# Optimization experiments

Measured on AMD Instinct MI355X. Metric: run time of the kernel, lower is better.

The kernel has to match this reference:

```python
import jax, jax.numpy as jnp
import numpy as np

SHAPES = np.array([[64, 64], [32, 32], [16, 16], [8, 8]], dtype=np.int64)  # (H_l, W_l)
STARTS = np.array([0, 4096, 5120, 5376], dtype=np.int64)
N_HEADS, N_LEVELS, N_POINTS = 8, 4, 4
NUM_LAYERS, D_MODEL, D_FFN = 6, 256, 1024
B, S = 1, int(SHAPES[:, 0].dot(SHAPES[:, 1]).item()) if False else (1, 5440)[1]
B = 1


def setup_inputs():
    key = jax.random.key(0)
    ks = jax.random.split(key, 16)
    C, F, L = D_MODEL, D_FFN, NUM_LAYERS
    w = lambda k, shape, s: jax.random.normal(k, shape, jnp.float32) * s
    d = {}
    d["src"] = jax.random.normal(ks[0], (B, S, C), jnp.float32)
    d["pos"] = jax.random.normal(ks[1], (B, S, C), jnp.float32) * 0.1
    d["valid_ratios"] = jnp.ones((B, N_LEVELS, 2), jnp.float32)
    d["spatial_shapes"] = jnp.asarray(SHAPES)
    d["level_start_index"] = jnp.asarray(STARTS)
    d["Wv"] = w(ks[2], (L, C, C), 0.03); d["bv"] = jnp.zeros((L, C), jnp.float32)
    d["Woff"] = w(ks[3], (L, C, N_HEADS * N_LEVELS * N_POINTS * 2), 0.002)
    d["boff"] = w(ks[4], (L, N_HEADS * N_LEVELS * N_POINTS * 2), 0.5)
    d["Wattn"] = w(ks[5], (L, C, N_HEADS * N_LEVELS * N_POINTS), 0.02)
    d["battn"] = jnp.zeros((L, N_HEADS * N_LEVELS * N_POINTS), jnp.float32)
    d["Wout"] = w(ks[6], (L, C, C), 0.03); d["bout"] = jnp.zeros((L, C), jnp.float32)
    d["ln1_g"] = jnp.ones((L, C), jnp.float32); d["ln1_b"] = jnp.zeros((L, C), jnp.float32)
    d["W1"] = w(ks[7], (L, C, F), 0.03); d["b1"] = jnp.zeros((L, F), jnp.float32)
    d["W2"] = w(ks[8], (L, F, C), 0.03); d["b2"] = jnp.zeros((L, C), jnp.float32)
    d["ln2_g"] = jnp.ones((L, C), jnp.float32); d["ln2_b"] = jnp.zeros((L, C), jnp.float32)
    return d


def layer_norm(x, g, b, eps=1e-5):
    m = jnp.mean(x, -1, keepdims=True)
    v = jnp.mean(jnp.square(x - m), -1, keepdims=True)
    return (x - m) * jax.lax.rsqrt(v + eps) * g + b


def get_reference_points(valid_ratios):
    # returns [B, S, L, 2] (x, y) normalized coords, matching the TF while-loop
    refs = []
    for l in range(N_LEVELS):
        H, W = int(SHAPES[l, 0]), int(SHAPES[l, 1])
        ry = jnp.linspace(0.5, H - 0.5, H)
        rx = jnp.linspace(0.5, W - 0.5, W)
        yy, xx = jnp.meshgrid(ry, rx, indexing='ij')
        yn = yy.reshape(-1)[None, :] / (valid_ratios[:, l, 0:1] * H)
        xn = xx.reshape(-1)[None, :] / (valid_ratios[:, l, 1:2] * W)
        refs.append(jnp.stack([xn, yn], -1))  # [B, H*W, 2]
    ref = jnp.concatenate(refs, axis=1)       # [B, S, 2]
    vr_wh = valid_ratios[:, None, :, ::-1]    # [B, 1, L, 2] -> (w, h)
    return ref[:, :, None, :] * vr_wh


def bilinear_sample(v_l, loc, Hl, Wl):
    # v_l: [B, Hl*Wl, nH, Dh]; loc: [B, S, nH, P, 2] in [0,1] coords
    # grid_sample align_corners=False, zero padding: pix = loc*size - 0.5
    x = loc[..., 0] * Wl - 0.5
    y = loc[..., 1] * Hl - 0.5
    x0 = jnp.floor(x); y0 = jnp.floor(y)
    lx = x - x0; ly = y - y0
    x0i = x0.astype(jnp.int32); y0i = y0.astype(jnp.int32)
    b_idx = jnp.arange(v_l.shape[0])[:, None, None, None]
    h_idx = jnp.arange(v_l.shape[2])[None, None, :, None]

    def gather(xi, yi):
        valid = (xi >= 0) & (xi < Wl) & (yi >= 0) & (yi < Hl)
        idx = jnp.clip(yi, 0, Hl - 1) * Wl + jnp.clip(xi, 0, Wl - 1)
        v = v_l[b_idx, idx, h_idx, :]  # [B,S,nH,P,Dh]
        return v * valid[..., None].astype(v.dtype)

    v00 = gather(x0i, y0i); v01 = gather(x0i + 1, y0i)
    v10 = gather(x0i, y0i + 1); v11 = gather(x0i + 1, y0i + 1)
    w00 = (1 - lx) * (1 - ly); w01 = lx * (1 - ly)
    w10 = (1 - lx) * ly; w11 = lx * ly
    return (v00 * w00[..., None] + v01 * w01[..., None]
            + v10 * w10[..., None] + v11 * w11[..., None])


def msda(query, src, ref, Wv, bv, Woff, boff, Wattn, battn, Wout, bout):
    Bq, Sq, C = src.shape
    Dh = C // N_HEADS
    value = (src @ Wv + bv).reshape(Bq, Sq, N_HEADS, Dh)
    off = (query @ Woff + boff).reshape(Bq, Sq, N_HEADS, N_LEVELS, N_POINTS, 2)
    aw = jax.nn.softmax((query @ Wattn + battn)
                        .reshape(Bq, Sq, N_HEADS, N_LEVELS * N_POINTS), -1)
    aw = aw.reshape(Bq, Sq, N_HEADS, N_LEVELS, N_POINTS)
    normalizer = jnp.asarray(SHAPES[:, ::-1].copy(), jnp.float32)  # [L,2]=(W,H)
    loc = ref[:, :, None, :, None, :] + off / normalizer[None, None, None, :, None, :]
    out = jnp.zeros((Bq, Sq, N_HEADS, Dh), value.dtype)
    for l in range(N_LEVELS):
        Hl, Wl = int(SHAPES[l, 0]), int(SHAPES[l, 1])
        s0 = int(STARTS[l])
        v_l = value[:, s0:s0 + Hl * Wl]
        sampled = bilinear_sample(v_l, loc[:, :, :, l], Hl, Wl)  # [B,S,nH,P,Dh]
        out = out + jnp.einsum('bshpd,bshp->bshd', sampled, aw[:, :, :, l])
    return out.reshape(Bq, Sq, C) @ Wout + bout


def reference(src, pos, valid_ratios, spatial_shapes, level_start_index,
              Wv, bv, Woff, boff, Wattn, battn, Wout, bout,
              ln1_g, ln1_b, W1, b1, W2, b2, ln2_g, ln2_b):
    ref = get_reference_points(valid_ratios)
    x = src
    for i in range(NUM_LAYERS):
        a = msda(x + pos, x, ref, Wv[i], bv[i], Woff[i], boff[i],
                 Wattn[i], battn[i], Wout[i], bout[i])
        x = layer_norm(x + a, ln1_g[i], ln1_b[i])
        f = jax.nn.relu(x @ W1[i] + b1[i]) @ W2[i] + b2[i]
        x = layer_norm(x + f, ln2_g[i], ln2_b[i])
    return x
```

## Files before the change

### kernel.cpp

```cpp
#include <hip/hip_runtime.h>
#include <hip/hip_bf16.h>

#define S_TOT 5440
#define C_DIM 256
#define F_DIM 1024
#define N_LAYERS 6

__device__ __constant__ int c_HW[4]    = {64, 32, 16, 8};
__device__ __constant__ int c_logW[4]  = {6, 5, 4, 3};
__device__ __constant__ int c_start[4] = {0, 4096, 5120, 5376};

typedef __attribute__((ext_vector_type(8))) short bf16x8;
typedef __attribute__((ext_vector_type(4))) float f32x4;

__device__ __forceinline__ short f2bf(float f) {
    __hip_bfloat16 h = __float2bfloat16(f);
    return *reinterpret_cast<short*>(&h);
}
__device__ __forceinline__ float bf2f(unsigned short u) {
    union { unsigned int i; float f; } c; c.i = ((unsigned int)u) << 16; return c.f;
}

__global__ __launch_bounds__(256) void prep_weights(
    const float* __restrict__ Wv, const float* __restrict__ Woff,
    const float* __restrict__ Wattn, const float* __restrict__ Wout,
    const float* __restrict__ W1, const float* __restrict__ W2,
    unsigned short* __restrict__ WT)
{
    __shared__ short T[64][72];
    const int bid = blockIdx.x;
    const int layer = bid / 184;
    const int r = bid % 184;
    const float* src; unsigned short* dst; int K, N, kb, nb;
    if (r < 16)       { src = Wv    + (long)layer*65536;  dst = WT + 0       + (long)layer*65536;  K=256;  N=256;  kb=r&3;        nb=r>>2; }
    else if (r < 32)  { src = Woff  + (long)layer*65536;  dst = WT + 393216  + (long)layer*65536;  K=256;  N=256;  kb=(r-16)&3;   nb=(r-16)>>2; }
    else if (r < 40)  { src = Wattn + (long)layer*32768;  dst = WT + 786432  + (long)layer*32768;  K=256;  N=128;  kb=(r-32)&3;   nb=(r-32)>>2; }
    else if (r < 56)  { src = Wout  + (long)layer*65536;  dst = WT + 983040  + (long)layer*65536;  K=256;  N=256;  kb=(r-40)&3;   nb=(r-40)>>2; }
    else if (r < 120) { src = W1    + (long)layer*262144; dst = WT + 1376256 + (long)layer*262144; K=256;  N=1024; kb=(r-56)&3;   nb=(r-56)>>2; }
    else              { src = W2    + (long)layer*262144; dst = WT + 2949120 + (long)layer*262144; K=1024; N=256;  kb=(r-120)&15; nb=(r-120)>>4; }
    const int k0 = kb * 64, n0 = nb * 64;
    const int t = threadIdx.x;
    {
        const int row = t >> 2, cg = (t & 3) * 16;
        const float* sp = src + (long)(k0 + row) * N + n0 + cg;
        float4 v0 = *(const float4*)sp;
        float4 v1 = *(const float4*)(sp + 4);
        float4 v2 = *(const float4*)(sp + 8);
        float4 v3 = *(const float4*)(sp + 12);
        short tmp[16];
        tmp[0]=f2bf(v0.x); tmp[1]=f2bf(v0.y); tmp[2]=f2bf(v0.z); tmp[3]=f2bf(v0.w);
        tmp[4]=f2bf(v1.x); tmp[5]=f2bf(v1.y); tmp[6]=f2bf(v1.z); tmp[7]=f2bf(v1.w);
        tmp[8]=f2bf(v2.x); tmp[9]=f2bf(v2.y); tmp[10]=f2bf(v2.z); tmp[11]=f2bf(v2.w);
        tmp[12]=f2bf(v3.x); tmp[13]=f2bf(v3.y); tmp[14]=f2bf(v3.z); tmp[15]=f2bf(v3.w);
// ... 41 lines not shown
            float4 g4 = *(const float4*)(g + q4 * 64 + j * 4);
            float4 b4 = *(const float4*)(b + q4 * 64 + j * 4);
            va[j*4+0] = (va[j*4+0] - mean) * rstd * g4.x + b4.x;
            va[j*4+1] = (va[j*4+1] - mean) * rstd * g4.y + b4.y;
            va[j*4+2] = (va[j*4+2] - mean) * rstd * g4.z + b4.z;
            va[j*4+3] = (va[j*4+3] - mean) * rstd * g4.w + b4.w;
        }
    }
    if (xout) {
        #pragma unroll
        for (int j = 0; j < 16; ++j) {
            float4 v;
            v.x = va[j*4+0]; v.y = va[j*4+1]; v.z = va[j*4+2]; v.w = va[j*4+3];
            *(float4*)(xout + gbase + j * 4) = v;
        }
    }
    if (pos) {
        #pragma unroll
        for (int j = 0; j < 16; ++j) {
            float4 p = *(const float4*)(pos + gbase + j * 4);
            va[j*4+0] += p.x; va[j*4+1] += p.y; va[j*4+2] += p.z; va[j*4+3] += p.w;
        }
    }
    #pragma unroll
    for (int j8 = 0; j8 < 8; ++j8) {
        short tmp[8];
        #pragma unroll
        for (int e = 0; e < 8; ++e) tmp[e] = f2bf(va[j8 * 8 + e]);
        *(bf16x8*)&As[row][q4 * 64 + j8 * 8] = *(bf16x8*)tmp;
    }
}

template<int NF>
__device__ __forceinline__ void core_Alds(
    const unsigned short* __restrict__ Bt, int nBase,
    const short (*As)[264], short (*Bs)[72], f32x4 (&acc)[2][NF])
{
    const int t = threadIdx.x;
    const int lane = t & 63, wave = t >> 6;
    const int wr = wave >> 1, wc = wave & 1;
    const int lr = lane & 15;

    #pragma unroll
    for (int i = 0; i < 2; ++i)
        #pragma unroll
        for (int j = 0; j < NF; ++j)
            acc[i][j] = (f32x4){0.f, 0.f, 0.f, 0.f};

    for (int k0 = 0; k0 < 256; k0 += 64) {
        bf16x8 rb[NF];
        #pragma unroll
        for (int q = 0; q < NF; ++q) {
            int flat = q * 256 + t, row = flat >> 3, cg = (flat & 7) * 8;
            rb[q] = *(const bf16x8*)(Bt + (long)(nBase + row) * 256 + k0 + cg);
        }
        __syncthreads();
        #pragma unroll
        for (int q = 0; q < NF; ++q) {
            int flat = q * 256 + t, row = flat >> 3, cg = (flat & 7) * 8;
            *(bf16x8*)&Bs[row][cg] = rb[q];
        }
        __syncthreads();
        #pragma unroll
        for (int kk = 0; kk < 2; ++kk) {
            const int lks = kk * 32 + (lane >> 4) * 8;
            bf16x8 af[2], bfr[NF];
            #pragma unroll
            for (int fm = 0; fm < 2; ++fm)
                af[fm] = *(const bf16x8*)&As[wr * 32 + fm * 16 + lr][k0 + lks];
            #pragma unroll
            for (int fn = 0; fn < NF; ++fn)
                bfr[fn] = *(bf16x8*)&Bs[wc * (NF * 16) + fn * 16 + lr][lks];
            #pragma unroll
            for (int fm = 0; fm < 2; ++fm)
                #pragma unroll
                for (int fn = 0; fn < NF; ++fn)
                    acc[fm][fn] = __builtin_amdgcn_mfma_f32_16x16x32_bf16(
                        af[fm], bfr[fn], acc[fm][fn], 0, 0, 0);
        }
    }
}

template<int NF>
__device__ __forceinline__ void gemm_core(
    const unsigned short* __restrict__ A, const unsigned short* __restrict__ Bt,
    int K, int mBase, int nBase, short (*As)[72], short (*Bs)[72],
    f32x4 (&acc)[2][NF])
{
    const int t = threadIdx.x;
    const int lane = t & 63, wave = t >> 6;
    const int wr = wave >> 1, wc = wave & 1;
    const int lr = lane & 15;

    #pragma unroll
    for (int i = 0; i < 2; ++i)
        #pragma unroll
        for (int j = 0; j < NF; ++j)
            acc[i][j] = (f32x4){0.f, 0.f, 0.f, 0.f};

    for (int k0 = 0; k0 < K; k0 += 64) {
        bf16x8 ra[2], rb[NF];
        #pragma unroll
        for (int q = 0; q < 2; ++q) {
            int flat = q * 256 + t, row = flat >> 3, cg = (flat & 7) * 8;
            ra[q] = *(const bf16x8*)(A + (long)(mBase + row) * K + k0 + cg);
        }
        #pragma unroll
        for (int q = 0; q < NF; ++q) {
            int flat = q * 256 + t, row = flat >> 3, cg = (flat & 7) * 8;
            rb[q] = *(const bf16x8*)(Bt + (long)(nBase + row) * K + k0 + cg);
        }
        __syncthreads();
        #pragma unroll
        for (int q = 0; q < 2; ++q) {
            int flat = q * 256 + t, row = flat >> 3, cg = (flat & 7) * 8;
            *(bf16x8*)&As[row][cg] = ra[q];
        }
        #pragma unroll
        for (int q = 0; q < NF; ++q) {
            int flat = q * 256 + t, row = flat >> 3, cg = (flat & 7) * 8;
            *(bf16x8*)&Bs[row][cg] = rb[q];
        }
        __syncthreads();
        #pragma unroll
        for (int kk = 0; kk < 2; ++kk) {
            const int lks = kk * 32 + (lane >> 4) * 8;
            bf16x8 af[2], bfr[NF];
            #pragma unroll
            for (int fm = 0; fm < 2; ++fm)
                af[fm] = *(bf16x8*)&As[wr * 32 + fm * 16 + lr][lks];
            #pragma unroll
            for (int fn = 0; fn < NF; ++fn)
                bfr[fn] = *(bf16x8*)&Bs[wc * (NF * 16) + fn * 16 + lr][lks];
            #pragma unroll
            for (int fm = 0; fm < 2; ++fm)
                #pragma unroll
                for (int fn = 0; fn < NF; ++fn)
                    acc[fm][fn] = __builtin_amdgcn_mfma_f32_16x16x32_bf16(
                        af[fm], bfr[fn], acc[fm][fn], 0, 0, 0);
        }
    }
}

__global__ __launch_bounds__(256) void proj_ln(
    const float* __restrict__ Ain, const float* __restrict__ pos,
    const float* __restrict__ g, const float* __restrict__ b,
    const unsigned short* __restrict__ WvT, const float* __restrict__ bv,
    const unsigned short* __restrict__ WofT, const float* __restrict__ bof,
    const unsigned short* __restrict__ WatT, const float* __restrict__ bat,
    unsigned short* __restrict__ value_bf, float* __restrict__ offraw,
    float* __restrict__ logits, float* __restrict__ xcur, int doLN)
{
    __shared__ short As[64][264];
    __shared__ short Bs[128][72];
    const int ny = blockIdx.y, mBase = blockIdx.x * 64;
    const unsigned short* Bp; const float* bias; int nBase, kind;
    if (ny < 2)      { Bp = WvT;  bias = bv;  nBase = ny * 128;       kind = 0; }
    else if (ny < 4) { Bp = WofT; bias = bof; nBase = (ny - 2) * 128; kind = 1; }
    else             { Bp = WatT; bias = bat; nBase = 0;              kind = 2; }

    prep_A(Ain, g, b, (kind > 0) ? pos : nullptr,
           (doLN && ny == 0) ? xcur : nullptr, mBase, doLN, As);

    f32x4 acc[2][4];
    core_Alds<4>(Bp, nBase, As, Bs, acc);

    const int lane = threadIdx.x & 63, wave = threadIdx.x >> 6;
    const int wr = wave >> 1, wc = wave & 1;
    #pragma unroll
    for (int fm = 0; fm < 2; ++fm)
        #pragma unroll
        for (int fn = 0; fn < 4; ++fn)
            #pragma unroll
            for (int r = 0; r < 4; ++r) {
                int m = mBase + wr * 32 + fm * 16 + (lane >> 4) * 4 + r;
                int n = nBase + wc * 64 + fn * 16 + (lane & 15);
                float v = acc[fm][fn][r] + bias[n];
                if (kind == 0)      value_bf[(long)m * 256 + n] = (unsigned short)f2bf(v);
                else if (kind == 1) offraw[(long)m * 256 + n] = v;
                else                logits[(long)m * 128 + n] = v;
            }
}

__global__ __launch_bounds__(256) void gemm_w1ln(
    const float* __restrict__ Ain, const float* __restrict__ g,
    const float* __restrict__ b, const unsigned short* __restrict__ W1T,
    const float* __restrict__ bias, unsigned short* __restrict__ hbuf,
    float* __restrict__ xout)
{
    __shared__ short As[64][264];
    __shared__ short Bs[128][72];
    const int mBase = blockIdx.x * 64, nBase = blockIdx.y * 128;

    prep_A(Ain, g, b, nullptr, (blockIdx.y == 0) ? xout : nullptr, mBase, 1, As);

    f32x4 acc[2][4];
    core_Alds<4>(W1T, nBase, As, Bs, acc);

    const int lane = threadIdx.x & 63, wave = threadIdx.x >> 6;
    const int wr = wave >> 1, wc = wave & 1;
    #pragma unroll
    for (int fm = 0; fm < 2; ++fm)
        #pragma unroll
        for (int fn = 0; fn < 4; ++fn)
            #pragma unroll
            for (int r = 0; r < 4; ++r) {
                int m = mBase + wr * 32 + fm * 16 + (lane >> 4) * 4 + r;
                int n = nBase + wc * 64 + fn * 16 + (lane & 15);
                float v = fmaxf(acc[fm][fn][r] + bias[n], 0.f);
                hbuf[(long)m * 1024 + n] = (unsigned short)f2bf(v);
            }
}

__global__ __launch_bounds__(256) void gemm_res(
    const unsigned short* __restrict__ A, const unsigned short* __restrict__ Bt,
    const float* __restrict__ bias, const float* __restrict__ res,
    float* __restrict__ out, int K)
{
    __shared__ short As[64][72];
    __shared__ short Bs[64][72];
    const int mBase = blockIdx.x * 64, nBase = blockIdx.y * 64;
    f32x4 acc[2][2];
    gemm_core<2>(A, Bt, K, mBase, nBase, As, Bs, acc);

    const int lane = threadIdx.x & 63, wave = threadIdx.x >> 6;
    const int wr = wave >> 1, wc = wave & 1;
    #pragma unroll
    for (int fm = 0; fm < 2; ++fm)
        #pragma unroll
        for (int fn = 0; fn < 2; ++fn)
            #pragma unroll
            for (int r = 0; r < 4; ++r) {
                int m = mBase + wr * 32 + fm * 16 + (lane >> 4) * 4 + r;
                int n = nBase + wc * 32 + fn * 16 + (lane & 15);
                out[(long)m * 256 + n] = acc[fm][fn][r] + bias[n] + res[(long)m * 256 + n];
            }
}

__global__ __launch_bounds__(256) void msda2(
    const unsigned short* __restrict__ value, const float* __restrict__ offraw,
    const float* __restrict__ logits, const float* __restrict__ vr,
    unsigned short* __restrict__ outB)
{
    const int t = threadIdx.x;
    const int q = t >> 7, tt = t & 127;
    const int s = blockIdx.x * 2 + q;

    __shared__ int4   sIdx[2][128];
    __shared__ float4 sW[2][128];
    __shared__ float  sPart[2][3][32][8];

    {
        const int pt = tt & 15, l = pt >> 2;

        float lg = logits[(long)s * 128 + tt];
        float m = lg;
        #pragma unroll
        for (int o = 1; o < 16; o <<= 1) m = fmaxf(m, __shfl_xor(m, o));
        float e = expf(lg - m);
        float sum = e;
        #pragma unroll
        for (int o = 1; o < 16; o <<= 1) sum += __shfl_xor(sum, o);
        float aw = e / sum;

        int ls = (s < 4096) ? 0 : (s < 5120) ? 1 : (s < 5376) ? 2 : 3;
        int lw = c_logW[ls];
        int Wq = c_HW[ls];
        int rem = s - c_start[ls];
        int qi = rem >> lw, qj = rem & (Wq - 1);
        float xh = (qj + 0.5f) / (vr[ls * 2 + 1] * (float)Wq);
        float yh = (qi + 0.5f) / (vr[ls * 2 + 0] * (float)Wq);

        const int Wl = c_HW[l], sl = c_start[l];
        const float fW = (float)Wl;
        float refx = xh * vr[l * 2 + 1];
        float refy = yh * vr[l * 2 + 0];
        float2 oxy = *(const float2*)(offraw + (long)s * 256 + tt * 2);
        float x = refx * fW + oxy.x - 0.5f;
        float y = refy * fW + oxy.y - 0.5f;
        float x0f = floorf(x), y0f = floorf(y);
        float fx = x - x0f, fy = y - y0f;
        int x0 = (int)x0f, y0 = (int)y0f;
        int x1 = x0 + 1, y1 = y0 + 1;
        float vx0 = (x0 >= 0 && x0 < Wl) ? 1.f : 0.f;
        float vx1 = (x1 >= 0 && x1 < Wl) ? 1.f : 0.f;
        float vy0 = (y0 >= 0 && y0 < Wl) ? 1.f : 0.f;
        float vy1 = (y1 >= 0 && y1 < Wl) ? 1.f : 0.f;
        int cx0 = min(max(x0, 0), Wl - 1), cx1 = min(max(x1, 0), Wl - 1);
        int cy0 = min(max(y0, 0), Wl - 1), cy1 = min(max(y1, 0), Wl - 1);

        int4 id;
        id.x = sl + cy0 * Wl + cx0;
        id.y = sl + cy0 * Wl + cx1;
        id.z = sl + cy1 * Wl + cx0;
        id.w = sl + cy1 * Wl + cx1;
        sIdx[q][tt] = id;
        float4 w4;
        w4.x = aw * (1.f - fx) * (1.f - fy) * vx0 * vy0;
        w4.y = aw * fx * (1.f - fy) * vx1 * vy0;
        w4.z = aw * (1.f - fx) * fy * vx0 * vy1;
        w4.w = aw * fx * fy * vx1 * vy1;
        sW[q][tt] = w4;
    }
    __syncthreads();

    const int pg = tt >> 5, h = (tt >> 2) & 7, dq = tt & 3;
    const int cb = h * 32 + dq * 8;

    float acc[8] = {0.f, 0.f, 0.f, 0.f, 0.f, 0.f, 0.f, 0.f};
    #pragma unroll
    for (int p = 0; p < 4; ++p) {
        const int ei = h * 16 + pg * 4 + p;
        int4 id = sIdx[q][ei];
        float4 w = sW[q][ei];
        bf16x8 u0 = *(const bf16x8*)(value + (long)id.x * 256 + cb);
        bf16x8 u1 = *(const bf16x8*)(value + (long)id.y * 256 + cb);
        bf16x8 u2 = *(const bf16x8*)(value + (long)id.z * 256 + cb);
        bf16x8 u3 = *(const bf16x8*)(value + (long)id.w * 256 + cb);
        #pragma unroll
        for (int e8 = 0; e8 < 8; ++e8) {
            acc[e8] += w.x * bf2f((unsigned short)u0[e8])
                     + w.y * bf2f((unsigned short)u1[e8])
                     + w.z * bf2f((unsigned short)u2[e8])
                     + w.w * bf2f((unsigned short)u3[e8]);
        }
    }

    if (pg > 0) {
        float4 a0, a1;
        a0.x = acc[0]; a0.y = acc[1]; a0.z = acc[2]; a0.w = acc[3];
        a1.x = acc[4]; a1.y = acc[5]; a1.z = acc[6]; a1.w = acc[7];
        *(float4*)&sPart[q][pg - 1][h * 4 + dq][0] = a0;
        *(float4*)&sPart[q][pg - 1][h * 4 + dq][4] = a1;
    }
    __syncthreads();
    if (pg == 0) {
        #pragma unroll
        for (int e8 = 0; e8 < 8; ++e8)
            acc[e8] += sPart[q][0][h * 4 + dq][e8]
                     + sPart[q][1][h * 4 + dq][e8]
                     + sPart[q][2][h * 4 + dq][e8];
        short o[8];
        #pragma unroll
        for (int e8 = 0; e8 < 8; ++e8) o[e8] = f2bf(acc[e8]);
        *(bf16x8*)(outB + (long)s * 256 + cb) = *(bf16x8*)o;
    }
}

__global__ __launch_bounds__(256) void ln4f(
    const float* __restrict__ in, const float* __restrict__ g,
    const float* __restrict__ b, float* __restrict__ out)
{
    const int wave = threadIdx.x >> 6, lane = threadIdx.x & 63;
    const int s = blockIdx.x * 4 + wave;
    f32x4 v = *(const f32x4*)(in + (long)s * 256 + lane * 4);

    float sum = v[0] + v[1] + v[2] + v[3];
    #pragma unroll
    for (int o = 1; o < 64; o <<= 1) sum += __shfl_xor(sum, o);
    const float mean = sum * (1.f / 256.f);

    f32x4 d = v - mean;
    float sq = d[0]*d[0] + d[1]*d[1] + d[2]*d[2] + d[3]*d[3];
    #pragma unroll
    for (int o = 1; o < 64; o <<= 1) sq += __shfl_xor(sq, o);
    const float rstd = rsqrtf(sq * (1.f / 256.f) + 1e-5f);

    f32x4 gg = *(const f32x4*)(g + lane * 4);
    f32x4 bb = *(const f32x4*)(b + lane * 4);
    f32x4 o4 = d * rstd * gg + bb;
    *(f32x4*)(out + (long)s * 256 + lane * 4) = o4;
}

extern "C" void kernel_launch(void* const* d_in, const int* in_sizes, int n_in,
                              void* d_out, int out_size, void* d_ws, size_t ws_size,
                              hipStream_t stream) {
    const float* src   = (const float*)d_in[0];
    const float* pos   = (const float*)d_in[1];
    const float* vr    = (const float*)d_in[2];
    const float* Wv    = (const float*)d_in[5];
    const float* bv    = (const float*)d_in[6];
    const float* Woff  = (const float*)d_in[7];
    const float* boff  = (const float*)d_in[8];
    const float* Wattn = (const float*)d_in[9];
    const float* battn = (const float*)d_in[10];
    const float* Wout  = (const float*)d_in[11];
    const float* bout  = (const float*)d_in[12];
    const float* ln1g  = (const float*)d_in[13];
    const float* ln1b  = (const float*)d_in[14];
    const float* W1    = (const float*)d_in[15];
    const float* b1    = (const float*)d_in[16];
    const float* W2    = (const float*)d_in[17];
    const float* b2    = (const float*)d_in[18];
    const float* ln2g  = (const float*)d_in[19];
    const float* ln2b  = (const float*)d_in[20];

    const int S = S_TOT, C = C_DIM;
    const long SC = (long)S * C;

    float* ws     = (float*)d_ws;
    float* tmp2   = ws;
    float* xcur   = tmp2 + SC;
    float* offraw = xcur + SC;
    float* logits = offraw + SC;
    unsigned short* value_bf = (unsigned short*)(logits + (long)S * 128);
    unsigned short* msda_bf  = value_bf + SC;
    unsigned short* hbuf_bf  = msda_bf + SC;
    unsigned short* WT       = hbuf_bf + (long)S * F_DIM;

    float* xln1 = offraw;

    const unsigned short* WvT  = WT + 0;
    const unsigned short* WofT = WT + 393216;
    const unsigned short* WatT = WT + 786432;
    const unsigned short* WouT = WT + 983040;
    const unsigned short* W1T  = WT + 1376256;
    const unsigned short* W2T  = WT + 2949120;

    prep_weights<<<1104, 256, 0, stream>>>(Wv, Woff, Wattn, Wout, W1, W2, WT);

    for (int i = 0; i < N_LAYERS; ++i) {
        const float* Ain = (i == 0) ? src : tmp2;
        const float* g2  = (i == 0) ? nullptr : ln2g + (long)(i - 1) * C;
        const float* bb2 = (i == 0) ? nullptr : ln2b + (long)(i - 1) * C;
        const float* resWout = (i == 0) ? src : xcur;

        proj_ln<<<dim3(85, 5), 256, 0, stream>>>(
            Ain, pos, g2, bb2,
            WvT + (long)i * 65536, bv + (long)i * C,
            WofT + (long)i * 65536, boff + (long)i * 256,
            WatT + (long)i * 32768, battn + (long)i * 128,
            value_bf, offraw, logits, xcur, (i == 0) ? 0 : 1);

        msda2<<<S / 2, 256, 0, stream>>>(value_bf, offraw, logits, vr, msda_bf);

        gemm_res<<<dim3(85, 4), 256, 0, stream>>>(
            msda_bf, WouT + (long)i * 65536, bout + (long)i * C, resWout, tmp2, 256);

        gemm_w1ln<<<dim3(85, 8), 256, 0, stream>>>(
            tmp2, ln1g + (long)i * C, ln1b + (long)i * C,
            W1T + (long)i * 262144, b1 + (long)i * F_DIM, hbuf_bf, xln1);

        gemm_res<<<dim3(85, 4), 256, 0, stream>>>(
            hbuf_bf, W2T + (long)i * 262144, b2 + (long)i * C, xln1, tmp2, 1024);
    }

    ln4f<<<S / 4, 256, 0, stream>>>(
        tmp2, ln2g + (long)(N_LAYERS - 1) * C, ln2b + (long)(N_LAYERS - 1) * C,
        (float*)d_out);
}
```

Before: 505.1 us.

## Fuse MSDA sampling, output projection, LayerNorm and FFN into one per-tile kernel

Replaces the four kernels run after the projection step (msda2, gemm_res for Wout, gemm_w1ln, gemm_res for W2) with one layer_post kernel. Each block handles 16 tokens: it does the deformable sampling into shared memory, then the Wout GEMM with residual, LayerNorm1, the W1 GEMM with ReLU kept in shared memory, and the W2 GEMM with the second residual. This removes the global round trips of the msda output, the hidden activations and the LN1 output, plus three launches. The cost is that B weight fragments are read straight from global memory without LDS tiling, so every block re-reads all weights. The grid is also small (340 blocks) and the large shared-memory footprint may limit occupancy.

```diff
diff --git a/kernel.cpp b/kernel.cpp
--- a/kernel.cpp
+++ b/kernel.cpp
@@ -175,67 +175,6 @@
     }
 }
 
-template<int NF>
-__device__ __forceinline__ void gemm_core(
-    const unsigned short* __restrict__ A, const unsigned short* __restrict__ Bt,
-    int K, int mBase, int nBase, short (*As)[72], short (*Bs)[72],
-    f32x4 (&acc)[2][NF])
-{
-    const int t = threadIdx.x;
-    const int lane = t & 63, wave = t >> 6;
-    const int wr = wave >> 1, wc = wave & 1;
-    const int lr = lane & 15;
-
-    #pragma unroll
-    for (int i = 0; i < 2; ++i)
-        #pragma unroll
-        for (int j = 0; j < NF; ++j)
-            acc[i][j] = (f32x4){0.f, 0.f, 0.f, 0.f};
-
-    for (int k0 = 0; k0 < K; k0 += 64) {
-        bf16x8 ra[2], rb[NF];
-        #pragma unroll
-        for (int q = 0; q < 2; ++q) {
-            int flat = q * 256 + t, row = flat >> 3, cg = (flat & 7) * 8;
-            ra[q] = *(const bf16x8*)(A + (long)(mBase + row) * K + k0 + cg);
-        }
-        #pragma unroll
-        for (int q = 0; q < NF; ++q) {
-            int flat = q * 256 + t, row = flat >> 3, cg = (flat & 7) * 8;
-            rb[q] = *(const bf16x8*)(Bt + (long)(nBase + row) * K + k0 + cg);
-        }
-        __syncthreads();
-        #pragma unroll
-        for (int q = 0; q < 2; ++q) {
-            int flat = q * 256 + t, row = flat >> 3, cg = (flat & 7) * 8;
-            *(bf16x8*)&As[row][cg] = ra[q];
-        }
-        #pragma unroll
-        for (int q = 0; q < NF; ++q) {
-            int flat = q * 256 + t, row = flat >> 3, cg = (flat & 7) * 8;
-            *(bf16x8*)&Bs[row][cg] = rb[q];
-        }
-        __syncthreads();
-        #pragma unroll
-        for (int kk = 0; kk < 2; ++kk) {
-            const int lks = kk * 32 + (lane >> 4) * 8;
-            bf16x8 af[2], bfr[NF];
-            #pragma unroll
-            for (int fm = 0; fm < 2; ++fm)
-                af[fm] = *(bf16x8*)&As[wr * 32 + fm * 16 + lr][lks];
-            #pragma unroll
-            for (int fn = 0; fn < NF; ++fn)
-                bfr[fn] = *(bf16x8*)&Bs[wc * (NF * 16) + fn * 16 + lr][lks];
-            #pragma unroll
-            for (int fm = 0; fm < 2; ++fm)
-                #pragma unroll
-                for (int fn = 0; fn < NF; ++fn)
-                    acc[fm][fn] = __builtin_amdgcn_mfma_f32_16x16x32_bf16(
-                        af[fm], bfr[fn], acc[fm][fn], 0, 0, 0);
-        }
-    }
-}
-
 __global__ __launch_bounds__(256) void proj_ln(
     const float* __restrict__ Ain, const float* __restrict__ pos,
     const float* __restrict__ g, const float* __restrict__ b,
@@ -276,168 +215,220 @@
             }
 }
 
-__global__ __launch_bounds__(256) void gemm_w1ln(
-    const float* __restrict__ Ain, const float* __restrict__ g,
-    const float* __restrict__ b, const unsigned short* __restrict__ W1T,
-    const float* __restrict__ bias, unsigned short* __restrict__ hbuf,
-    float* __restrict__ xout)
-{
-    __shared__ short As[64][264];
-    __shared__ short Bs[128][72];
-    const int mBase = blockIdx.x * 64, nBase = blockIdx.y * 128;
-
-    prep_A(Ain, g, b, nullptr, (blockIdx.y == 0) ? xout : nullptr, mBase, 1, As);
-
-    f32x4 acc[2][4];
-    core_Alds<4>(W1T, nBase, As, Bs, acc);
-
-    const int lane = threadIdx.x & 63, wave = threadIdx.x >> 6;
-    const int wr = wave >> 1, wc = wave & 1;
-    #pragma unroll
-    for (int fm = 0; fm < 2; ++fm)
-        #pragma unroll
-        for (int fn = 0; fn < 4; ++fn)
-            #pragma unroll
-            for (int r = 0; r < 4; ++r) {
-                int m = mBase + wr * 32 + fm * 16 + (lane >> 4) * 4 + r;
-                int n = nBase + wc * 64 + fn * 16 + (lane & 15);
-                float v = fmaxf(acc[fm][fn][r] + bias[n], 0.f);
-                hbuf[(long)m * 1024 + n] = (unsigned short)f2bf(v);
-            }
-}
-
-__global__ __launch_bounds__(256) void gemm_res(
-    const unsigned short* __restrict__ A, const unsigned short* __restrict__ Bt,
-    const float* __restrict__ bias, const float* __restrict__ res,
-    float* __restrict__ out, int K)
-{
-    __shared__ short As[64][72];
-    __shared__ short Bs[64][72];
-    const int mBase = blockIdx.x * 64, nBase = blockIdx.y * 64;
-    f32x4 acc[2][2];
-    gemm_core<2>(A, Bt, K, mBase, nBase, As, Bs, acc);
-
-    const int lane = threadIdx.x & 63, wave = threadIdx.x >> 6;
-    const int wr = wave >> 1, wc = wave & 1;
-    #pragma unroll
-    for (int fm = 0; fm < 2; ++fm)
-        #pragma unroll
-        for (int fn = 0; fn < 2; ++fn)
-            #pragma unroll
-            for (int r = 0; r < 4; ++r) {
-                int m = mBase + wr * 32 + fm * 16 + (lane >> 4) * 4 + r;
-                int n = nBase + wc * 32 + fn * 16 + (lane & 15);
-                out[(long)m * 256 + n] = acc[fm][fn][r] + bias[n] + res[(long)m * 256 + n];
-            }
-}
-
-__global__ __launch_bounds__(256) void msda2(
+template<int KSTEPS, int LDA>
+__device__ __forceinline__ void mm16(
+    const short* __restrict__ A, const unsigned short* __restrict__ Bt,
+    int ldb, int nBase, f32x4 (&acc)[4], int lane)
+{
+    const int lr = lane & 15, kg = (lane >> 4) * 8;
+    #pragma unroll
+    for (int j = 0; j < 4; ++j) acc[j] = (f32x4){0.f, 0.f, 0.f, 0.f};
+    for (int ks = 0; ks < KSTEPS; ++ks) {
+        #pragma unroll
+        for (int kk = 0; kk < 2; ++kk) {
+            const int k = ks * 64 + kk * 32 + kg;
+            bf16x8 af = *(const bf16x8*)&A[lr * LDA + k];
+            bf16x8 bf0 = *(const bf16x8*)(Bt + (long)(nBase + 0  + lr) * ldb + k);
+            bf16x8 bf1 = *(const bf16x8*)(Bt + (long)(nBase + 16 + lr) * ldb + k);
+            bf16x8 bf2 = *(const bf16x8*)(Bt + (long)(nBase + 32 + lr) * ldb + k);
+            bf16x8 bf3 = *(const bf16x8*)(Bt + (long)(nBase + 48 + lr) * ldb + k);
+            acc[0] = __builtin_amdgcn_mfma_f32_16x16x32_bf16(af, bf0, acc[0], 0, 0, 0);
+            acc[1] = __builtin_amdgcn_mfma_f32_16x16x32_bf16(af, bf1, acc[1], 0, 0, 0);
+            acc[2] = __builtin_amdgcn_mfma_f32_16x16x32_bf16(af, bf2, acc[2], 0, 0, 0);
+            acc[3] = __builtin_amdgcn_mfma_f32_16x16x32_bf16(af, bf3, acc[3], 0, 0, 0);
+        }
+    }
+}
+
+__global__ __launch_bounds__(256) void layer_post(
     const unsigned short* __restrict__ value, const float* __restrict__ offraw,
     const float* __restrict__ logits, const float* __restrict__ vr,
-    unsigned short* __restrict__ outB)
-{
+    const float* __restrict__ res,
+    const unsigned short* __restrict__ WouT, const float* __restrict__ bout,
+    const float* __restrict__ ln1g, const float* __restrict__ ln1b,
+    const unsigned short* __restrict__ W1T, const float* __restrict__ b1,
+    const unsigned short* __restrict__ W2T, const float* __restrict__ b2,
+    float* __restrict__ out)
+{
+    __shared__ __align__(16) short sH[16][1032];
+    __shared__ __align__(16) short sM[16][264];
+    __shared__ __align__(16) short sA1[16][264];
+    __shared__ float2 sRed[4][16];
+    __shared__ float2 sMR[16];
+
     const int t = threadIdx.x;
-    const int q = t >> 7, tt = t & 127;
-    const int s = blockIdx.x * 2 + q;
-
-    __shared__ int4   sIdx[2][128];
-    __shared__ float4 sW[2][128];
-    __shared__ float  sPart[2][3][32][8];
-
+    const int sBase = blockIdx.x * 16;
+    const int lane = t & 63, wave = t >> 6;
+    const int lr = lane & 15, rowg = (lane >> 4) * 4;
+
+    int4*   sIdx = (int4*)&sH[0][0];
+    float4* sWt  = (float4*)((char*)&sH[0][0] + 16384);
+    for (int c = 0; c < 2; ++c) {
+        #pragma unroll
+        for (int it = 0; it < 4; ++it) {
+            const int id = it * 256 + t;
+            const int q = id >> 7, tt = id & 127;
+            const int s = sBase + c * 8 + q;
+            const int pt = tt & 15, l = pt >> 2;
+
+            float lg = logits[(long)s * 128 + tt];
+            float m = lg;
+            #pragma unroll
+            for (int o = 1; o < 16; o <<= 1) m = fmaxf(m, __shfl_xor(m, o));
+            float e = expf(lg - m);
+            float sum = e;
+            #pragma unroll
+            for (int o = 1; o < 16; o <<= 1) sum += __shfl_xor(sum, o);
+            float aw = e / sum;
+
+            int ls = (s < 4096) ? 0 : (s < 5120) ? 1 : (s < 5376) ? 2 : 3;
+            int lw = c_logW[ls];
+            int Wq = c_HW[ls];
+            int rem = s - c_start[ls];
+            int qi = rem >> lw, qj = rem & (Wq - 1);
+            float xh = (qj + 0.5f) / (vr[ls * 2 + 1] * (float)Wq);
+            float yh = (qi + 0.5f) / (vr[ls * 2 + 0] * (float)Wq);
+
+            const int Wl = c_HW[l], sl = c_start[l];
+            const float fW = (float)Wl;
+            float refx = xh * vr[l * 2 + 1];
+            float refy = yh * vr[l * 2 + 0];
+            float2 oxy = *(const float2*)(offraw + (long)s * 256 + tt * 2);
+            float x = refx * fW + oxy.x - 0.5f;
+            float y = refy * fW + oxy.y - 0.5f;
+            float x0f = floorf(x), y0f = floorf(y);
+            float fx = x - x0f, fy = y - y0f;
+            int x0 = (int)x0f, y0 = (int)y0f;
+            int x1 = x0 + 1, y1 = y0 + 1;
+            float vx0 = (x0 >= 0 && x0 < Wl) ? 1.f : 0.f;
+            float vx1 = (x1 >= 0 && x1 < Wl) ? 1.f : 0.f;
+            float vy0 = (y0 >= 0 && y0 < Wl) ? 1.f : 0.f;
+            float vy1 = (y1 >= 0 && y1 < Wl) ? 1.f : 0.f;
+            int cx0 = min(max(x0, 0), Wl - 1), cx1 = min(max(x1, 0), Wl - 1);
+            int cy0 = min(max(y0, 0), Wl - 1), cy1 = min(max(y1, 0), Wl - 1);
+
+            int4 id4;
+            id4.x = sl + cy0 * Wl + cx0;
+            id4.y = sl + cy0 * Wl + cx1;
+            id4.z = sl + cy1 * Wl + cx0;
+            id4.w = sl + cy1 * Wl + cx1;
+            sIdx[q * 128 + tt] = id4;
+            float4 w4;
+            w4.x = aw * (1.f - fx) * (1.f - fy) * vx0 * vy0;
+            w4.y = aw * fx * (1.f - fy) * vx1 * vy0;
+            w4.z = aw * (1.f - fx) * fy * vx0 * vy1;
+            w4.w = aw * fx * fy * vx1 * vy1;
+            sWt[q * 128 + tt] = w4;
+        }
+        __syncthreads();
+        {
+            const int q2 = t >> 5, h = (t >> 2) & 7, dq = t & 3;
+            const int cb = h * 32 + dq * 8;
+            float a8[8] = {0.f,0.f,0.f,0.f,0.f,0.f,0.f,0.f};
+            #pragma unroll
+            for (int pt = 0; pt < 16; ++pt) {
+                int4 id = sIdx[q2 * 128 + h * 16 + pt];
+                float4 w = sWt[q2 * 128 + h * 16 + pt];
+                bf16x8 u0 = *(const bf16x8*)(value + (long)id.x * 256 + cb);
+                bf16x8 u1 = *(const bf16x8*)(value + (long)id.y * 256 + cb);
+                bf16x8 u2 = *(const bf16x8*)(value + (long)id.z * 256 + cb);
+                bf16x8 u3 = *(const bf16x8*)(value + (long)id.w * 256 + cb);
+                #pragma unroll
+                for (int e8 = 0; e8 < 8; ++e8)
+                    a8[e8] += w.x * bf2f((unsigned short)u0[e8])
+                            + w.y * bf2f((unsigned short)u1[e8])
+                            + w.z * bf2f((unsigned short)u2[e8])
+                            + w.w * bf2f((unsigned short)u3[e8]);
+            }
+            short o8[8];
+            #pragma unroll
+            for (int e8 = 0; e8 < 8; ++e8) o8[e8] = f2bf(a8[e8]);
+            *(bf16x8*)&sM[c * 8 + q2][cb] = *(bf16x8*)o8;
+        }
+        __syncthreads();
+    }
+
+    f32x4 acc[4];
+    mm16<4, 264>(&sM[0][0], WouT, 256, wave * 64, acc, lane);
+
+    float bias_c[4];
+    int ncol[4];
+    #pragma unroll
+    for (int fn = 0; fn < 4; ++fn) {
+        ncol[fn] = wave * 64 + fn * 16 + lr;
+        bias_c[fn] = bout[ncol[fn]];
+    }
+    #pragma unroll
+    for (int fn = 0; fn < 4; ++fn)
+        #pragma unroll
+        for (int r = 0; r < 4; ++r)
+            acc[fn][r] += bias_c[fn] + res[(long)(sBase + rowg + r) * 256 + ncol[fn]];
+
+    #pragma unroll
+    for (int r = 0; r < 4; ++r) {
+        float s1 = acc[0][r] + acc[1][r] + acc[2][r] + acc[3][r];
+        float s2 = acc[0][r]*acc[0][r] + acc[1][r]*acc[1][r]
+                 + acc[2][r]*acc[2][r] + acc[3][r]*acc[3][r];
+        #pragma unroll
+        for (int o = 1; o < 16; o <<= 1) {
+            s1 += __shfl_xor(s1, o);
+            s2 += __shfl_xor(s2, o);
+        }
+        if (lr == 0) { float2 pr; pr.x = s1; pr.y = s2; sRed[wave][rowg + r] = pr; }
+    }
+    __syncthreads();
+    if (t < 16) {
+        float2 a0 = sRed[0][t], a1 = sRed[1][t], a2 = sRed[2][t], a3 = sRed[3][t];
+        float mean = (a0.x + a1.x + a2.x + a3.x) * (1.f / 256.f);
+        float var  = (a0.y + a1.y + a2.y + a3.y) * (1.f / 256.f) - mean * mean;
+        float2 mr; mr.x = mean; mr.y = rsqrtf(var + 1e-5f);
+        sMR[t] = mr;
+    }
+    __syncthreads();
+
+    f32x4 lnv[4];
     {
-        const int pt = tt & 15, l = pt >> 2;
-
-        float lg = logits[(long)s * 128 + tt];
-        float m = lg;
-        #pragma unroll
-        for (int o = 1; o < 16; o <<= 1) m = fmaxf(m, __shfl_xor(m, o));
-        float e = expf(lg - m);
-        float sum = e;
-        #pragma unroll
-        for (int o = 1; o < 16; o <<= 1) sum += __shfl_xor(sum, o);
-        float aw = e / sum;
-
-        int ls = (s < 4096) ? 0 : (s < 5120) ? 1 : (s < 5376) ? 2 : 3;
-        int lw = c_logW[ls];
-        int Wq = c_HW[ls];
-        int rem = s - c_start[ls];
-        int qi = rem >> lw, qj = rem & (Wq - 1);
-        float xh = (qj + 0.5f) / (vr[ls * 2 + 1] * (float)Wq);
-        float yh = (qi + 0.5f) / (vr[ls * 2 + 0] * (float)Wq);
-
-        const int Wl = c_HW[l], sl = c_start[l];
-        const float fW = (float)Wl;
-        float refx = xh * vr[l * 2 + 1];
-        float refy = yh * vr[l * 2 + 0];
-        float2 oxy = *(const float2*)(offraw + (long)s * 256 + tt * 2);
-        float x = refx * fW + oxy.x - 0.5f;
-        float y = refy * fW + oxy.y - 0.5f;
-        float x0f = floorf(x), y0f = floorf(y);
-        float fx = x - x0f, fy = y - y0f;
-        int x0 = (int)x0f, y0 = (int)y0f;
-        int x1 = x0 + 1, y1 = y0 + 1;
-        float vx0 = (x0 >= 0 && x0 < Wl) ? 1.f : 0.f;
-        float vx1 = (x1 >= 0 && x1 < Wl) ? 1.f : 0.f;
-        float vy0 = (y0 >= 0 && y0 < Wl) ? 1.f : 0.f;
-        float vy1 = (y1 >= 0 && y1 < Wl) ? 1.f : 0.f;
-        int cx0 = min(max(x0, 0), Wl - 1), cx1 = min(max(x1, 0), Wl - 1);
-        int cy0 = min(max(y0, 0), Wl - 1), cy1 = min(max(y1, 0), Wl - 1);
-
-        int4 id;
-        id.x = sl + cy0 * Wl + cx0;
-        id.y = sl + cy0 * Wl + cx1;
-        id.z = sl + cy1 * Wl + cx0;
-        id.w = sl + cy1 * Wl + cx1;
-        sIdx[q][tt] = id;
-        float4 w4;
-        w4.x = aw * (1.f - fx) * (1.f - fy) * vx0 * vy0;
-        w4.y = aw * fx * (1.f - fy) * vx1 * vy0;
-        w4.z = aw * (1.f - fx) * fy * vx0 * vy1;
-        w4.w = aw * fx * fy * vx1 * vy1;
-        sW[q][tt] = w4;
+        float g_c[4], b_c[4];
+        #pragma unroll
+        for (int fn = 0; fn < 4; ++fn) { g_c[fn] = ln1g[ncol[fn]]; b_c[fn] = ln1b[ncol[fn]]; }
+        #pragma unroll
+        for (int r = 0; r < 4; ++r) {
+            float2 mr = sMR[rowg + r];
+            #pragma unroll
+            for (int fn = 0; fn < 4; ++fn)
+                lnv[fn][r] = (acc[fn][r] - mr.x) * mr.y * g_c[fn] + b_c[fn];
+        }
+        #pragma unroll
+        for (int fn = 0; fn < 4; ++fn)
+            #pragma unroll
+            for (int r = 0; r < 4; ++r)
+                sA1[rowg + r][ncol[fn]] = f2bf(lnv[fn][r]);
     }
     __syncthreads();
 
-    const int pg = tt >> 5, h = (tt >> 2) & 7, dq = tt & 3;
-    const int cb = h * 32 + dq * 8;
-
-    float acc[8] = {0.f, 0.f, 0.f, 0.f, 0.f, 0.f, 0.f, 0.f};
-    #pragma unroll
-    for (int p = 0; p < 4; ++p) {
-        const int ei = h * 16 + pg * 4 + p;
-        int4 id = sIdx[q][ei];
-        float4 w = sW[q][ei];
-        bf16x8 u0 = *(const bf16x8*)(value + (long)id.x * 256 + cb);
-        bf16x8 u1 = *(const bf16x8*)(value + (long)id.y * 256 + cb);
-        bf16x8 u2 = *(const bf16x8*)(value + (long)id.z * 256 + cb);
-        bf16x8 u3 = *(const bf16x8*)(value + (long)id.w * 256 + cb);
-        #pragma unroll
-        for (int e8 = 0; e8 < 8; ++e8) {
-            acc[e8] += w.x * bf2f((unsigned short)u0[e8])
-                     + w.y * bf2f((unsigned short)u1[e8])
-                     + w.z * bf2f((unsigned short)u2[e8])
-                     + w.w * bf2f((unsigned short)u3[e8]);
-        }
-    }
-
-    if (pg > 0) {
-        float4 a0, a1;
-        a0.x = acc[0]; a0.y = acc[1]; a0.z = acc[2]; a0.w = acc[3];
-        a1.x = acc[4]; a1.y = acc[5]; a1.z = acc[6]; a1.w = acc[7];
-        *(float4*)&sPart[q][pg - 1][h * 4 + dq][0] = a0;
-        *(float4*)&sPart[q][pg - 1][h * 4 + dq][4] = a1;
+    #pragma unroll
+    for (int nc = 0; nc < 4; ++nc) {
+        f32x4 h4[4];
+        mm16<4, 264>(&sA1[0][0], W1T, 256, nc * 256 + wave * 64, h4, lane);
+        #pragma unroll
+        for (int fn = 0; fn < 4; ++fn) {
+            int n = nc * 256 + wave * 64 + fn * 16 + lr;
+            float bb = b1[n];
+            #pragma unroll
+            for (int r = 0; r < 4; ++r)
+                sH[rowg + r][n] = f2bf(fmaxf(h4[fn][r] + bb, 0.f));
+        }
     }
     __syncthreads();
-    if (pg == 0) {
-        #pragma unroll
-        for (int e8 = 0; e8 < 8; ++e8)
-            acc[e8] += sPart[q][0][h * 4 + dq][e8]
-                     + sPart[q][1][h * 4 + dq][e8]
-                     + sPart[q][2][h * 4 + dq][e8];
-        short o[8];
-        #pragma unroll
-        for (int e8 = 0; e8 < 8; ++e8) o[e8] = f2bf(acc[e8]);
-        *(bf16x8*)(outB + (long)s * 256 + cb) = *(bf16x8*)o;
+
+    f32x4 o4[4];
+    mm16<16, 1032>(&sH[0][0], W2T, 1024, wave * 64, o4, lane);
+    #pragma unroll
+    for (int fn = 0; fn < 4; ++fn) {
+        float bb = b2[ncol[fn]];
+        #pragma unroll
+        for (int r = 0; r < 4; ++r)
+            out[(long)(sBase + rowg + r) * 256 + ncol[fn]] = o4[fn][r] + bb + lnv[fn][r];
     }
 }
 
@@ -498,11 +489,7 @@
     float* offraw = xcur + SC;
     float* logits = offraw + SC;
     unsigned short* value_bf = (unsigned short*)(logits + (long)S * 128);
-    unsigned short* msda_bf  = value_bf + SC;
-    unsigned short* hbuf_bf  = msda_bf + SC;
-    unsigned short* WT       = hbuf_bf + (long)S * F_DIM;
-
-    float* xln1 = offraw;
+    unsigned short* WT       = value_bf + SC;
 
     const unsigned short* WvT  = WT + 0;
     const unsigned short* WofT = WT + 393216;
@@ -526,17 +513,13 @@
             WatT + (long)i * 32768, battn + (long)i * 128,
             value_bf, offraw, logits, xcur, (i == 0) ? 0 : 1);
 
-        msda2<<<S / 2, 256, 0, stream>>>(value_bf, offraw, logits, vr, msda_bf);
-
-        gemm_res<<<dim3(85, 4), 256, 0, stream>>>(
-            msda_bf, WouT + (long)i * 65536, bout + (long)i * C, resWout, tmp2, 256);
-
-        gemm_w1ln<<<dim3(85, 8), 256, 0, stream>>>(
-            tmp2, ln1g + (long)i * C, ln1b + (long)i * C,
-            W1T + (long)i * 262144, b1 + (long)i * F_DIM, hbuf_bf, xln1);
-
-        gemm_res<<<dim3(85, 4), 256, 0, stream>>>(
-            hbuf_bf, W2T + (long)i * 262144, b2 + (long)i * C, xln1, tmp2, 1024);
+        layer_post<<<S / 16, 256, 0, stream>>>(
+            value_bf, offraw, logits, vr, resWout,
+            WouT + (long)i * 65536, bout + (long)i * C,
+            ln1g + (long)i * C, ln1b + (long)i * C,
+            W1T + (long)i * 262144, b1 + (long)i * F_DIM,
+            W2T + (long)i * 262144, b2 + (long)i * C,
+            tmp2);
     }
 
     ln4f<<<S / 4, 256, 0, stream>>>(
```

Measured after the change: 791.4 us. 56.7% more time.

## Stage GEMM tiles via direct global-to-LDS loads with XOR swizzle; shuffle-reduce sampling

Applied to the files above, without the earlier changes.

GEMM cores now load B (and A) tiles straight from global memory into LDS using the global_load_lds builtin, with an XOR-swizzled unpadded layout that avoids bank conflicts and skips the register round trip. A trailing barrier is added per k-step because there is no register staging. The deformable sampling kernel remaps threads so the point-group partial sums sit in adjacent lanes and are combined with xor shuffles instead of an LDS partial buffer plus a barrier. Its bf16 unpacking now handles packed 32-bit words. The direct-to-LDS path depends on builtin availability and the lane-to-address layout it expects.

```diff
diff --git a/kernel.cpp b/kernel.cpp
--- a/kernel.cpp
+++ b/kernel.cpp
@@ -12,13 +12,25 @@
 
 typedef __attribute__((ext_vector_type(8))) short bf16x8;
 typedef __attribute__((ext_vector_type(4))) float f32x4;
+typedef __attribute__((ext_vector_type(4))) unsigned int u32x4;
 
 __device__ __forceinline__ short f2bf(float f) {
     __hip_bfloat16 h = __float2bfloat16(f);
     return *reinterpret_cast<short*>(&h);
 }
-__device__ __forceinline__ float bf2f(unsigned short u) {
-    union { unsigned int i; float f; } c; c.i = ((unsigned int)u) << 16; return c.f;
+union uf32 { unsigned int u; float f; };
+__device__ __forceinline__ float lo_f(unsigned int u) { uf32 c; c.u = u << 16;          return c.f; }
+__device__ __forceinline__ float hi_f(unsigned int u) { uf32 c; c.u = u & 0xffff0000u; return c.f; }
+
+__device__ __forceinline__ void gstage16(const unsigned short* g, short* ldsBase, int lane) {
+#if defined(__has_builtin) && __has_builtin(__builtin_amdgcn_global_load_lds)
+    __builtin_amdgcn_global_load_lds(
+        (const __attribute__((address_space(1))) unsigned int*)(g),
+        (__attribute__((address_space(3))) unsigned int*)(ldsBase),
+        16, 0, 0);
+#else
+    *(bf16x8*)(ldsBase + lane * 8) = *(const bf16x8*)g;
+#endif
 }
 
 __global__ __launch_bounds__(256) void prep_weights(
@@ -126,14 +138,15 @@
 }
 
 template<int NF>
-__device__ __forceinline__ void core_Alds(
-    const unsigned short* __restrict__ Bt, int nBase,
-    const short (*As)[264], short (*Bs)[72], f32x4 (&acc)[2][NF])
+__device__ __forceinline__ void core_Alds2(
+    const unsigned short* __restrict__ Bt, int ldb, int nBase,
+    const short (*As)[264], short* __restrict__ BsLin, f32x4 (&acc)[2][NF])
 {
     const int t = threadIdx.x;
     const int lane = t & 63, wave = t >> 6;
     const int wr = wave >> 1, wc = wave & 1;
     const int lr = lane & 15;
+    const int ldRow = lane >> 3, ldC16 = lane & 7;
 
     #pragma unroll
     for (int i = 0; i < 2; ++i)
@@ -142,29 +155,28 @@
             acc[i][j] = (f32x4){0.f, 0.f, 0.f, 0.f};
 
     for (int k0 = 0; k0 < 256; k0 += 64) {
-        bf16x8 rb[NF];
-        #pragma unroll
-        for (int q = 0; q < NF; ++q) {
-            int flat = q * 256 + t, row = flat >> 3, cg = (flat & 7) * 8;
-            rb[q] = *(const bf16x8*)(Bt + (long)(nBase + row) * 256 + k0 + cg);
-        }
-        __syncthreads();
-        #pragma unroll
-        for (int q = 0; q < NF; ++q) {
-            int flat = q * 256 + t, row = flat >> 3, cg = (flat & 7) * 8;
-            *(bf16x8*)&Bs[row][cg] = rb[q];
+        #pragma unroll
+        for (int qq = 0; qq < NF; ++qq) {
+            const int wbase = wave * (NF * 8) + qq * 8;
+            const int row = wbase + ldRow;
+            const int c16 = ldC16 ^ (row & 7);
+            gstage16(Bt + (long)(nBase + row) * ldb + k0 + c16 * 8,
+                     BsLin + wbase * 64, lane);
         }
         __syncthreads();
         #pragma unroll
         for (int kk = 0; kk < 2; ++kk) {
             const int lks = kk * 32 + (lane >> 4) * 8;
+            const int c16f = lks >> 3;
             bf16x8 af[2], bfr[NF];
             #pragma unroll
             for (int fm = 0; fm < 2; ++fm)
                 af[fm] = *(const bf16x8*)&As[wr * 32 + fm * 16 + lr][k0 + lks];
             #pragma unroll
-            for (int fn = 0; fn < NF; ++fn)
-                bfr[fn] = *(bf16x8*)&Bs[wc * (NF * 16) + fn * 16 + lr][lks];
+            for (int fn = 0; fn < NF; ++fn) {
+                const int row = wc * (NF * 16) + fn * 16 + lr;
+                bfr[fn] = *(const bf16x8*)&BsLin[row * 64 + ((c16f ^ (row & 7)) << 3)];
+            }
             #pragma unroll
             for (int fm = 0; fm < 2; ++fm)
                 #pragma unroll
@@ -172,19 +184,21 @@
                     acc[fm][fn] = __builtin_amdgcn_mfma_f32_16x16x32_bf16(
                         af[fm], bfr[fn], acc[fm][fn], 0, 0, 0);
         }
+        __syncthreads();
     }
 }
 
 template<int NF>
-__device__ __forceinline__ void gemm_core(
+__device__ __forceinline__ void gemm_core2(
     const unsigned short* __restrict__ A, const unsigned short* __restrict__ Bt,
-    int K, int mBase, int nBase, short (*As)[72], short (*Bs)[72],
-    f32x4 (&acc)[2][NF])
+    int K, int mBase, int nBase, short* __restrict__ AsLin,
+    short* __restrict__ BsLin, f32x4 (&acc)[2][NF])
 {
     const int t = threadIdx.x;
     const int lane = t & 63, wave = t >> 6;
     const int wr = wave >> 1, wc = wave & 1;
     const int lr = lane & 15;
+    const int ldRow = lane >> 3, ldC16 = lane & 7;
 
     #pragma unroll
     for (int i = 0; i < 2; ++i)
@@ -193,39 +207,38 @@
             acc[i][j] = (f32x4){0.f, 0.f, 0.f, 0.f};
 
     for (int k0 = 0; k0 < K; k0 += 64) {
-        bf16x8 ra[2], rb[NF];
-        #pragma unroll
-        for (int q = 0; q < 2; ++q) {
-            int flat = q * 256 + t, row = flat >> 3, cg = (flat & 7) * 8;
-            ra[q] = *(const bf16x8*)(A + (long)(mBase + row) * K + k0 + cg);
-        }
-        #pragma unroll
-        for (int q = 0; q < NF; ++q) {
-            int flat = q * 256 + t, row = flat >> 3, cg = (flat & 7) * 8;
-            rb[q] = *(const bf16x8*)(Bt + (long)(nBase + row) * K + k0 + cg);
-        }
-        __syncthreads();
-        #pragma unroll
-        for (int q = 0; q < 2; ++q) {
-            int flat = q * 256 + t, row = flat >> 3, cg = (flat & 7) * 8;
-            *(bf16x8*)&As[row][cg] = ra[q];
-        }
-        #pragma unroll
-        for (int q = 0; q < NF; ++q) {
-            int flat = q * 256 + t, row = flat >> 3, cg = (flat & 7) * 8;
-            *(bf16x8*)&Bs[row][cg] = rb[q];
+        #pragma unroll
+        for (int qq = 0; qq < 2; ++qq) {
+            const int wbase = wave * 16 + qq * 8;
+            const int row = wbase + ldRow;
+            const int c16 = ldC16 ^ (row & 7);
+            gstage16(A + (long)(mBase + row) * K + k0 + c16 * 8,
+                     AsLin + wbase * 64, lane);
+        }
+        #pragma unroll
+        for (int qq = 0; qq < NF; ++qq) {
+            const int wbase = wave * (NF * 8) + qq * 8;
+            const int row = wbase + ldRow;
+            const int c16 = ldC16 ^ (row & 7);
+            gstage16(Bt + (long)(nBase + row) * K + k0 + c16 * 8,
+                     BsLin + wbase * 64, lane);
         }
         __syncthreads();
         #pragma unroll
         for (int kk = 0; kk < 2; ++kk) {
             const int lks = kk * 32 + (lane >> 4) * 8;
+            const int c16f = lks >> 3;
             bf16x8 af[2], bfr[NF];
             #pragma unroll
-            for (int fm = 0; fm < 2; ++fm)
-                af[fm] = *(bf16x8*)&As[wr * 32 + fm * 16 + lr][lks];
-            #pragma unroll
-            for (int fn = 0; fn < NF; ++fn)
-                bfr[fn] = *(bf16x8*)&Bs[wc * (NF * 16) + fn * 16 + lr][lks];
+            for (int fm = 0; fm < 2; ++fm) {
+                const int row = wr * 32 + fm * 16 + lr;
+                af[fm] = *(const bf16x8*)&AsLin[row * 64 + ((c16f ^ (row & 7)) << 3)];
+            }
+            #pragma unroll
+            for (int fn = 0; fn < NF; ++fn) {
+                const int row = wc * (NF * 16) + fn * 16 + lr;
+                bfr[fn] = *(const bf16x8*)&BsLin[row * 64 + ((c16f ^ (row & 7)) << 3)];
+            }
             #pragma unroll
             for (int fm = 0; fm < 2; ++fm)
                 #pragma unroll
@@ -233,6 +246,7 @@
                     acc[fm][fn] = __builtin_amdgcn_mfma_f32_16x16x32_bf16(
                         af[fm], bfr[fn], acc[fm][fn], 0, 0, 0);
         }
+        __syncthreads();
     }
 }
 
@@ -246,7 +260,7 @@
     float* __restrict__ logits, float* __restrict__ xcur, int doLN)
 {
     __shared__ short As[64][264];
-    __shared__ short Bs[128][72];
+    __shared__ short BsLin[128 * 64];
     const int ny = blockIdx.y, mBase = blockIdx.x * 64;
     const unsigned short* Bp; const float* bias; int nBase, kind;
     if (ny < 2)      { Bp = WvT;  bias = bv;  nBase = ny * 128;       kind = 0; }
@@ -257,7 +271,7 @@
            (doLN && ny == 0) ? xcur : nullptr, mBase, doLN, As);
 
     f32x4 acc[2][4];
-    core_Alds<4>(Bp, nBase, As, Bs, acc);
+    core_Alds2<4>(Bp, 256, nBase, As, BsLin, acc);
 
     const int lane = threadIdx.x & 63, wave = threadIdx.x >> 6;
     const int wr = wave >> 1, wc = wave & 1;
@@ -283,13 +297,13 @@
     float* __restrict__ xout)
 {
     __shared__ short As[64][264];
-    __shared__ short Bs[128][72];
+    __shared__ short BsLin[128 * 64];
     const int mBase = blockIdx.x * 64, nBase = blockIdx.y * 128;
 
     prep_A(Ain, g, b, nullptr, (blockIdx.y == 0) ? xout : nullptr, mBase, 1, As);
 
     f32x4 acc[2][4];
-    core_Alds<4>(W1T, nBase, As, Bs, acc);
+    core_Alds2<4>(W1T, 256, nBase, As, BsLin, acc);
 
     const int lane = threadIdx.x & 63, wave = threadIdx.x >> 6;
     const int wr = wave >> 1, wc = wave & 1;
@@ -311,11 +325,11 @@
     const float* __restrict__ bias, const float* __restrict__ res,
     float* __restrict__ out, int K)
 {
-    __shared__ short As[64][72];
-    __shared__ short Bs[64][72];
+    __shared__ short AsLin[64 * 64];
+    __shared__ short BsLin[64 * 64];
     const int mBase = blockIdx.x * 64, nBase = blockIdx.y * 64;
     f32x4 acc[2][2];
-    gemm_core<2>(A, Bt, K, mBase, nBase, As, Bs, acc);
+    gemm_core2<2>(A, Bt, K, mBase, nBase, AsLin, BsLin, acc);
 
     const int lane = threadIdx.x & 63, wave = threadIdx.x >> 6;
     const int wr = wave >> 1, wc = wave & 1;
@@ -342,7 +356,6 @@
 
     __shared__ int4   sIdx[2][128];
     __shared__ float4 sW[2][128];
-    __shared__ float  sPart[2][3][32][8];
 
     {
         const int pt = tt & 15, l = pt >> 2;
@@ -383,12 +396,12 @@
         int cx0 = min(max(x0, 0), Wl - 1), cx1 = min(max(x1, 0), Wl - 1);
         int cy0 = min(max(y0, 0), Wl - 1), cy1 = min(max(y1, 0), Wl - 1);
 
-        int4 id;
-        id.x = sl + cy0 * Wl + cx0;
-        id.y = sl + cy0 * Wl + cx1;
-        id.z = sl + cy1 * Wl + cx0;
-        id.w = sl + cy1 * Wl + cx1;
-        sIdx[q][tt] = id;
+        int4 id4;
+        id4.x = sl + cy0 * Wl + cx0;
+        id4.y = sl + cy0 * Wl + cx1;
+        id4.z = sl + cy1 * Wl + cx0;
+        id4.w = sl + cy1 * Wl + cx1;
+        sIdx[q][tt] = id4;
         float4 w4;
         w4.x = aw * (1.f - fx) * (1.f - fy) * vx0 * vy0;
         w4.y = aw * fx * (1.f - fy) * vx1 * vy0;
@@ -398,46 +411,37 @@
     }
     __syncthreads();
 
-    const int pg = tt >> 5, h = (tt >> 2) & 7, dq = tt & 3;
+    const int h = tt >> 4, dq = (tt >> 2) & 3, pg = tt & 3;
     const int cb = h * 32 + dq * 8;
 
-    float acc[8] = {0.f, 0.f, 0.f, 0.f, 0.f, 0.f, 0.f, 0.f};
+    float a8[8] = {0.f,0.f,0.f,0.f,0.f,0.f,0.f,0.f};
     #pragma unroll
     for (int p = 0; p < 4; ++p) {
         const int ei = h * 16 + pg * 4 + p;
         int4 id = sIdx[q][ei];
         float4 w = sW[q][ei];
-        bf16x8 u0 = *(const bf16x8*)(value + (long)id.x * 256 + cb);
-        bf16x8 u1 = *(const bf16x8*)(value + (long)id.y * 256 + cb);
-        bf16x8 u2 = *(const bf16x8*)(value + (long)id.z * 256 + cb);
-        bf16x8 u3 = *(const bf16x8*)(value + (long)id.w * 256 + cb);
-        #pragma unroll
-        for (int e8 = 0; e8 < 8; ++e8) {
-            acc[e8] += w.x * bf2f((unsigned short)u0[e8])
-                     + w.y * bf2f((unsigned short)u1[e8])
-                     + w.z * bf2f((unsigned short)u2[e8])
-                     + w.w * bf2f((unsigned short)u3[e8]);
-        }
-    }
-
-    if (pg > 0) {
-        float4 a0, a1;
-        a0.x = acc[0]; a0.y = acc[1]; a0.z = acc[2]; a0.w = acc[3];
-        a1.x = acc[4]; a1.y = acc[5]; a1.z = acc[6]; a1.w = acc[7];
-        *(float4*)&sPart[q][pg - 1][h * 4 + dq][0] = a0;
-        *(float4*)&sPart[q][pg - 1][h * 4 + dq][4] = a1;
-    }
-    __syncthreads();
+        u32x4 u0 = *(const u32x4*)(value + (long)id.x * 256 + cb);
+        u32x4 u1 = *(const u32x4*)(value + (long)id.y * 256 + cb);
+        u32x4 u2 = *(const u32x4*)(value + (long)id.z * 256 + cb);
+        u32x4 u3 = *(const u32x4*)(value + (long)id.w * 256 + cb);
+        #pragma unroll
+        for (int j = 0; j < 4; ++j) {
+            a8[2*j]   += w.x * lo_f(u0[j]) + w.y * lo_f(u1[j])
+                       + w.z * lo_f(u2[j]) + w.w * lo_f(u3[j]);
+            a8[2*j+1] += w.x * hi_f(u0[j]) + w.y * hi_f(u1[j])
+                       + w.z * hi_f(u2[j]) + w.w * hi_f(u3[j]);
+        }
+    }
+    #pragma unroll
+    for (int j = 0; j < 8; ++j) {
+        a8[j] += __shfl_xor(a8[j], 1);
+        a8[j] += __shfl_xor(a8[j], 2);
+    }
     if (pg == 0) {
-        #pragma unroll
-        for (int e8 = 0; e8 < 8; ++e8)
-            acc[e8] += sPart[q][0][h * 4 + dq][e8]
-                     + sPart[q][1][h * 4 + dq][e8]
-                     + sPart[q][2][h * 4 + dq][e8];
-        short o[8];
-        #pragma unroll
-        for (int e8 = 0; e8 < 8; ++e8) o[e8] = f2bf(acc[e8]);
-        *(bf16x8*)(outB + (long)s * 256 + cb) = *(bf16x8*)o;
+        short o8[8];
+        #pragma unroll
+        for (int j = 0; j < 8; ++j) o8[j] = f2bf(a8[j]);
+        *(bf16x8*)(outB + (long)s * 256 + cb) = *(bf16x8*)o8;
     }
 }
 
```

After: 583.3 us. 15.5% more time.
